# Optimization experiments

Hardware: AMD Instinct MI355X
Metric: run time of the kernel (lower is better)

Reference implementation:

```python
import jax, jax.numpy as jnp
import numpy as np

N = 100000
E = 1600000
G = 2048          # number of graphs in the batch
HEADS = 4
HID = 16          # per-head channels
IN_CH = 128
D = HEADS * HID   # 64, concat output width per layer
NEG_SLOPE = 0.2


def _gat_layer(x, src, dst, W, a_src, a_dst, bias):
    # x: [N, Fin], W: [Fin, H*C], a_src/a_dst: [H, C], bias: [H*C]
    h = (x @ W).reshape(N, HEADS, HID)                      # [N, H, C]
    al_s = jnp.einsum('nhc,hc->nh', h, a_src)               # [N, H]
    al_d = jnp.einsum('nhc,hc->nh', h, a_dst)               # [N, H]
    e = jax.nn.leaky_relu(al_s[src] + al_d[dst], NEG_SLOPE) # [E+N, H]
    # segment softmax over incoming edges of each destination node
    m = jax.ops.segment_max(e, dst, num_segments=N)         # [N, H]
    e = jnp.exp(e - m[dst])
    s = jax.ops.segment_sum(e, dst, num_segments=N)
    alpha = e / (s[dst] + 1e-16)                            # [E+N, H]
    msg = h[src] * alpha[..., None]                         # [E+N, H, C]
    out = jax.ops.segment_sum(msg, dst, num_segments=N)     # [N, H, C]
    return out.reshape(N, D) + bias


def setup_inputs() -> dict:
    key = jax.random.key(0)
    ks = jax.random.split(key, 16)
    x = jax.random.normal(ks[0], (N, IN_CH), dtype=jnp.float32)
    edge_index = jax.random.randint(ks[1], (2, E), 0, N, dtype=jnp.int64)
    batch = jnp.sort(jax.random.randint(ks[2], (N,), 0, G, dtype=jnp.int64))
    inp = {'x': x, 'edge_index': edge_index, 'batch': batch}
    fins = [IN_CH, D, D]
    for i, fin in enumerate(fins):
        kk = jax.random.split(ks[3 + i], 4)
        sc = 1.0 / np.sqrt(fin)
        inp[f'W{i}'] = jax.random.normal(kk[0], (fin, D), dtype=jnp.float32) * sc
        inp[f'as{i}'] = jax.random.normal(kk[1], (HEADS, HID), dtype=jnp.float32) * 0.1
        inp[f'ad{i}'] = jax.random.normal(kk[2], (HEADS, HID), dtype=jnp.float32) * 0.1
        inp[f'b{i}'] = jnp.zeros((D,), dtype=jnp.float32)
    inp['head_w'] = jax.random.normal(ks[10], (1, D), dtype=jnp.float32) * (1.0 / np.sqrt(D))
    inp['head_b'] = jnp.zeros((1,), dtype=jnp.float32)
    return inp


def reference(x, edge_index, batch,
              W0, as0, ad0, b0,
              W1, as1, ad1, b1,
              W2, as2, ad2, b2,
              head_w, head_b):
    # PyG GATConv adds self-loops by default
    loops = jnp.arange(N, dtype=edge_index.dtype)
    src = jnp.concatenate([edge_index[0], loops])
    dst = jnp.concatenate([edge_index[1], loops])
    layers = [(W0, as0, ad0, b0), (W1, as1, ad1, b1), (W2, as2, ad2, b2)]
    h = x.astype(jnp.float32)
    for (W, a_s, a_d, b) in layers:
        h = _gat_layer(h, src, dst, W, a_s, a_d, b)
        h = jax.nn.relu(h)  # dropout p=0.0 -> identity
    pooled = jax.ops.segment_sum(h, batch, num_segments=G)  # [G, D]
    out = pooled @ head_w.T + head_b                         # [G, 1]
    return out.reshape(-1)                                   # out_dim == 1 -> flatten
```

## Files before the change

### kernel.cpp

```cpp
#include <hip/hip_runtime.h>
#include <hip/hip_bf16.h>
#include <hip/hip_fp16.h>
#include <cstdint>
#include <cstddef>

#define NN 100000
#define EE 1600000
#define GG 2048

constexpr int NB_SCAN = (NN + 255) / 256;

__device__ __forceinline__ float lrelu(float v) { return v > 0.f ? v : 0.2f * v; }

__global__ void k_count(const int* __restrict__ ei, int* __restrict__ deg,
                        int* __restrict__ rank) {
    int i = blockIdx.x * blockDim.x + threadIdx.x;
    if (i >= EE + NN) return;
    int d = (i < EE) ? ei[EE + i] : (i - EE);
    rank[i] = atomicAdd(&deg[d], 1);
}

__global__ void k_scan1(const int* __restrict__ deg, int* __restrict__ offs,
                        int* __restrict__ bsums) {
    __shared__ int tmp[256];
    int tid = threadIdx.x;
    int i = blockIdx.x * 256 + tid;
    int v = (i < NN) ? deg[i] : 0;
    tmp[tid] = v; __syncthreads();
    for (int off = 1; off < 256; off <<= 1) {
        int t = (tid >= off) ? tmp[tid - off] : 0;
        __syncthreads();
        tmp[tid] += t;
        __syncthreads();
    }
    if (i < NN) offs[i] = tmp[tid] - v;
    if (tid == 255) bsums[blockIdx.x] = tmp[255];
}

__global__ void k_scan2(int* __restrict__ bsums) {
    __shared__ int tmp[512];
    int tid = threadIdx.x;
    int v = (tid < NB_SCAN) ? bsums[tid] : 0;
    tmp[tid] = v; __syncthreads();
    for (int off = 1; off < 512; off <<= 1) {
        int t = (tid >= off) ? tmp[tid - off] : 0;
        __syncthreads();
        tmp[tid] += t;
        __syncthreads();
    }
    if (tid < NB_SCAN) bsums[tid] = tmp[tid] - v;
}

__global__ void k_scan3(int* __restrict__ offs, const int* __restrict__ bsums) {
    int i = blockIdx.x * 256 + threadIdx.x;
    if (i < NN) offs[i] += bsums[blockIdx.x];
}

__global__ void k_scatter(const int* __restrict__ ei, const int* __restrict__ offs,
                          const int* __restrict__ rank, int* __restrict__ col) {
    int i = blockIdx.x * blockDim.x + threadIdx.x;
    if (i >= EE + NN) return;
    int s, d;
    if (i < EE) { s = ei[i]; d = ei[EE + i]; } else { s = d = i - EE; }
    col[offs[d] + rank[i]] = s;
}

template <int FIN>
__global__ __launch_bounds__(256) void k_gemm(const float* __restrict__ X,
                                              const float* __restrict__ W,
                                              const float* __restrict__ asrc,
                                              const float* __restrict__ adst,
                                              float* __restrict__ H,
                                              float* __restrict__ als,
                                              float* __restrict__ ald) {
    int j  = threadIdx.x & 63;
    int ty = threadIdx.x >> 6;
    int row = __builtin_amdgcn_readfirstlane(blockIdx.x * 16 + ty * 4);
    const float* x0 = X + (size_t)row * FIN;
    const float* x1 = x0 + FIN;
    const float* x2 = x1 + FIN;
    const float* x3 = x2 + FIN;
    float a0 = 0.f, a1 = 0.f, a2 = 0.f, a3 = 0.f;
#pragma unroll
    for (int k = 0; k < FIN; k += 4) {
        float4 xa = *(const float4*)(x0 + k);
        float4 xb = *(const float4*)(x1 + k);
        float4 xc = *(const float4*)(x2 + k);
        float4 xd = *(const float4*)(x3 + k);
        float w0 = W[(k + 0) * 64 + j];
        float w1 = W[(k + 1) * 64 + j];
        float w2 = W[(k + 2) * 64 + j];
        float w3 = W[(k + 3) * 64 + j];
        a0 += xa.x * w0 + xa.y * w1 + xa.z * w2 + xa.w * w3;
        a1 += xb.x * w0 + xb.y * w1 + xb.z * w2 + xb.w * w3;
        a2 += xc.x * w0 + xc.y * w1 + xc.z * w2 + xc.w * w3;
        a3 += xd.x * w0 + xd.y * w1 + xd.z * w2 + xd.w * w3;
    }
    H[(size_t)(row + 0) * 64 + j] = a0;
    H[(size_t)(row + 1) * 64 + j] = a1;
    H[(size_t)(row + 2) * 64 + j] = a2;
    H[(size_t)(row + 3) * 64 + j] = a3;
    float asj = asrc[j], adj = adst[j];
    float accs[4] = {a0, a1, a2, a3};
#pragma unroll
    for (int r = 0; r < 4; r++) {
        float vs = accs[r] * asj;
        float vd = accs[r] * adj;
#pragma unroll
        for (int off = 8; off > 0; off >>= 1) {
            vs += __shfl_xor(vs, off, 64);
            vd += __shfl_xor(vd, off, 64);
        }
        if ((j & 15) == 0) {
            int h = j >> 4;
            als[(size_t)(row + r) * 4 + h] = vs;
            ald[(size_t)(row + r) * 4 + h] = vd;
        }
    }
}

#define LWPITCH 260
__global__ __launch_bounds__(256) void k_agg(
    const float* __restrict__ H, const float* __restrict__ als,
    const float* __restrict__ ald, const int* __restrict__ offs,
    const int* __restrict__ deg, const int* __restrict__ col,
    const float* __restrict__ bias, float* __restrict__ Hout,
    const int* __restrict__ batch, const float* __restrict__ hw,
    float* __restrict__ out, int last) {
    __shared__ float lws[16 * LWPITCH];
    __shared__ int   lsi[16][64];
    int tid = threadIdx.x;
    int g = tid >> 4;
    int l = tid & 15;
    int n = blockIdx.x * 16 + g;
    int start = offs[n];
    int len = deg[n];
    float4 ad4 = ((const float4*)ald)[n];
    int hsel = l >> 2;
    const float4* Hp = (const float4*)H + l;
    float* lw = lws + g * LWPITCH;
    bool fast = (len <= 64);
    float inv = 1.f;

    if (fast) {
        float ev[4][4];
        int   si[4];
        bool  vld[4];
        float m0 = -1e30f, m1 = -1e30f, m2 = -1e30f, m3 = -1e30f;
#pragma unroll
        for (int it = 0; it < 4; it++) {
            int e = l + it * 16;
            vld[it] = (e < len);
            int s = vld[it] ? col[start + e] : 0;
            si[it] = s;
            float4 a = ((const float4*)als)[s];
            ev[it][0] = lrelu(a.x + ad4.x); ev[it][1] = lrelu(a.y + ad4.y);
            ev[it][2] = lrelu(a.z + ad4.z); ev[it][3] = lrelu(a.w + ad4.w);
            if (vld[it]) {
                m0 = fmaxf(m0, ev[it][0]); m1 = fmaxf(m1, ev[it][1]);
                m2 = fmaxf(m2, ev[it][2]); m3 = fmaxf(m3, ev[it][3]);
            }
        }
#pragma unroll
        for (int off = 8; off > 0; off >>= 1) {
            m0 = fmaxf(m0, __shfl_xor(m0, off, 16));
            m1 = fmaxf(m1, __shfl_xor(m1, off, 16));
            m2 = fmaxf(m2, __shfl_xor(m2, off, 16));
            m3 = fmaxf(m3, __shfl_xor(m3, off, 16));
        }
        float s0 = 0.f, s1 = 0.f, s2 = 0.f, s3 = 0.f;
#pragma unroll
        for (int it = 0; it < 4; it++) {
            int e = l + it * 16;
            float w0 = vld[it] ? __expf(ev[it][0] - m0) : 0.f;
            float w1 = vld[it] ? __expf(ev[it][1] - m1) : 0.f;
            float w2 = vld[it] ? __expf(ev[it][2] - m2) : 0.f;
            float w3 = vld[it] ? __expf(ev[it][3] - m3) : 0.f;
            s0 += w0; s1 += w1; s2 += w2; s3 += w3;
            ((float4*)(lw + e * 4))[0] = make_float4(w0, w1, w2, w3);
            lsi[g][e] = vld[it] ? si[it] : 0;
        }
#pragma unroll
        for (int off = 8; off > 0; off >>= 1) {
            s0 += __shfl_xor(s0, off, 16); s1 += __shfl_xor(s1, off, 16);
            s2 += __shfl_xor(s2, off, 16); s3 += __shfl_xor(s3, off, 16);
        }
        float smh = hsel == 0 ? s0 : hsel == 1 ? s1 : hsel == 2 ? s2 : s3;
        inv = 1.f / (smh + 1e-16f);
    }

    __syncthreads();

    float4 acc = {0.f, 0.f, 0.f, 0.f};
    if (fast) {
        int e = 0;
        for (; e + 4 <= len; e += 4) {
            int sa = lsi[g][e], sb = lsi[g][e + 1], sc = lsi[g][e + 2], sd = lsi[g][e + 3];
            float wa = lw[(e + 0) * 4 + hsel];
            float wb = lw[(e + 1) * 4 + hsel];
            float wc = lw[(e + 2) * 4 + hsel];
            float wd = lw[(e + 3) * 4 + hsel];
            float4 ha = Hp[(size_t)sa * 16];
            float4 hb = Hp[(size_t)sb * 16];
            float4 hc = Hp[(size_t)sc * 16];
            float4 hd = Hp[(size_t)sd * 16];
            acc.x += wa * ha.x + wb * hb.x + wc * hc.x + wd * hd.x;
            acc.y += wa * ha.y + wb * hb.y + wc * hc.y + wd * hd.y;
            acc.z += wa * ha.z + wb * hb.z + wc * hc.z + wd * hd.z;
            acc.w += wa * ha.w + wb * hb.w + wc * hc.w + wd * hd.w;
        }
        for (; e < len; e++) {
            int sa = lsi[g][e];
            float wa = lw[e * 4 + hsel];
            float4 ha = Hp[(size_t)sa * 16];
            acc.x += wa * ha.x; acc.y += wa * ha.y;
            acc.z += wa * ha.z; acc.w += wa * ha.w;
        }
    } else {
        float m0 = -1e30f, m1 = -1e30f, m2 = -1e30f, m3 = -1e30f;
        for (int e = l; e < len; e += 16) {
            int s = col[start + e];
            float4 a = ((const float4*)als)[s];
            m0 = fmaxf(m0, lrelu(a.x + ad4.x)); m1 = fmaxf(m1, lrelu(a.y + ad4.y));
            m2 = fmaxf(m2, lrelu(a.z + ad4.z)); m3 = fmaxf(m3, lrelu(a.w + ad4.w));
        }
#pragma unroll
        for (int off = 8; off > 0; off >>= 1) {
            m0 = fmaxf(m0, __shfl_xor(m0, off, 16));
            m1 = fmaxf(m1, __shfl_xor(m1, off, 16));
            m2 = fmaxf(m2, __shfl_xor(m2, off, 16));
            m3 = fmaxf(m3, __shfl_xor(m3, off, 16));
        }
        float s0 = 0.f, s1 = 0.f, s2 = 0.f, s3 = 0.f;
        for (int e = l; e < len; e += 16) {
            int s = col[start + e];
            float4 a = ((const float4*)als)[s];
            s0 += __expf(lrelu(a.x + ad4.x) - m0); s1 += __expf(lrelu(a.y + ad4.y) - m1);
            s2 += __expf(lrelu(a.z + ad4.z) - m2); s3 += __expf(lrelu(a.w + ad4.w) - m3);
        }
#pragma unroll
        for (int off = 8; off > 0; off >>= 1) {
            s0 += __shfl_xor(s0, off, 16); s1 += __shfl_xor(s1, off, 16);
            s2 += __shfl_xor(s2, off, 16); s3 += __shfl_xor(s3, off, 16);
        }
        float mh = hsel == 0 ? m0 : hsel == 1 ? m1 : hsel == 2 ? m2 : m3;
        float sh = hsel == 0 ? s0 : hsel == 1 ? s1 : hsel == 2 ? s2 : s3;
        float ih = 1.f / (sh + 1e-16f);
        float ah = hsel == 0 ? ad4.x : hsel == 1 ? ad4.y : hsel == 2 ? ad4.z : ad4.w;
        for (int e = 0; e < len; e++) {
            int s = col[start + e];
            float alpha = __expf(lrelu(als[(size_t)s * 4 + hsel] + ah) - mh) * ih;
            float4 ha = Hp[(size_t)s * 16];
            acc.x += alpha * ha.x; acc.y += alpha * ha.y;
            acc.z += alpha * ha.z; acc.w += alpha * ha.w;
        }
        inv = 1.f;
    }

    float4 b4 = ((const float4*)bias)[l];
    float4 o4;
    o4.x = fmaxf(acc.x * inv + b4.x, 0.f);
    o4.y = fmaxf(acc.y * inv + b4.y, 0.f);
    o4.z = fmaxf(acc.z * inv + b4.z, 0.f);
    o4.w = fmaxf(acc.w * inv + b4.w, 0.f);
    if (!last) {
        ((float4*)Hout)[(size_t)n * 16 + l] = o4;
    } else {
        float4 w4 = ((const float4*)hw)[l];
        float t = o4.x * w4.x + o4.y * w4.y + o4.z * w4.z + o4.w * w4.w;
#pragma unroll
        for (int off = 8; off > 0; off >>= 1) t += __shfl_xor(t, off, 16);
        if (l == 0) atomicAdd(&out[batch[n]], t);
    }
}

__global__ void k_out_init(const float* __restrict__ head_b, float* __restrict__ out) {
    int g = blockIdx.x * blockDim.x + threadIdx.x;
    if (g < GG) out[g] = head_b[0];
}

extern "C" void kernel_launch(void* const* d_in, const int* in_sizes, int n_in,
                              void* d_out, int out_size, void* d_ws, size_t ws_size,
                              hipStream_t stream) {
    const float* x     = (const float*)d_in[0];
    const int*   ei    = (const int*)d_in[1];
    const int*   batch = (const int*)d_in[2];
    const float* Wm[3] = {(const float*)d_in[3], (const float*)d_in[7],  (const float*)d_in[11]};
    const float* As[3] = {(const float*)d_in[4], (const float*)d_in[8],  (const float*)d_in[12]};
    const float* Ad[3] = {(const float*)d_in[5], (const float*)d_in[9],  (const float*)d_in[13]};
    const float* Bb[3] = {(const float*)d_in[6], (const float*)d_in[10], (const float*)d_in[14]};
    const float* hw = (const float*)d_in[15];
    const float* hb = (const float*)d_in[16];
    float* out = (float*)d_out;

    uint8_t* w = (uint8_t*)d_ws;
    auto alloc = [&](size_t bytes) -> void* {
        void* p = (void*)w;
        w += (bytes + 255) & ~(size_t)255;
        return p;
    };
    float* H       = (float*)alloc((size_t)NN * 64 * 4);
    float* Bf      = (float*)alloc((size_t)NN * 64 * 4);
    float* als     = (float*)alloc((size_t)NN * 4 * 4);
    float* ald     = (float*)alloc((size_t)NN * 4 * 4);
    int*   deg     = (int*)alloc((size_t)NN * 4);
    int*   offs    = (int*)alloc((size_t)NN * 4);
    int*   rank    = (int*)alloc((size_t)(EE + NN) * 4);
    int*   col     = (int*)alloc((size_t)(EE + NN) * 4);
    int*   bsums   = (int*)alloc((size_t)((NB_SCAN + 63) & ~63) * 4);

    hipMemsetAsync(deg, 0, (size_t)NN * 4, stream);

    int eb = (EE + NN + 255) / 256;
    k_count  <<<eb, 256, 0, stream>>>(ei, deg, rank);
    k_scan1  <<<NB_SCAN, 256, 0, stream>>>(deg, offs, bsums);
    k_scan2  <<<1, 512, 0, stream>>>(bsums);
    k_scan3  <<<NB_SCAN, 256, 0, stream>>>(offs, bsums);
    k_scatter<<<eb, 256, 0, stream>>>(ei, offs, rank, col);
    k_out_init<<<(GG + 255) / 256, 256, 0, stream>>>(hb, out);

    const float* cur_in = x;
    for (int L = 0; L < 3; L++) {
        if (L == 0)
            k_gemm<128><<<NN / 16, 256, 0, stream>>>(
                cur_in, Wm[L], As[L], Ad[L], H, als, ald);
        else
            k_gemm<64><<<NN / 16, 256, 0, stream>>>(
                cur_in, Wm[L], As[L], Ad[L], H, als, ald);
        k_agg <<<NN / 16, 256, 0, stream>>>(
            H, als, ald, offs, deg, col, Bb[L], Bf, batch, hw, out, (L == 2) ? 1 : 0);
        cur_in = Bf;
    }
}
```

Before: 542.5 us.

## Single-pass GAT aggregation without max subtraction, dropping shared-memory staging

Replaces the two-phase aggregation (parallel max/exp into LDS, barrier, then gather) with one pass in which each lane computes its own exp weights and gathers neighbour features, eight edges at a time. The softmax max-subtraction is dropped, which relies on logits being small enough that exp does not overflow. LDS use and __syncthreads are removed and launch bounds ask for 6 blocks per CU, aiming at higher occupancy and more loads in flight. In exchange every lane redundantly reads col and als for each edge, and numerical stability depends on the input scale.

```diff
diff --git a/kernel.cpp b/kernel.cpp
--- a/kernel.cpp
+++ b/kernel.cpp
@@ -119,143 +119,53 @@
     }
 }
 
-#define LWPITCH 260
-__global__ __launch_bounds__(256) void k_agg(
+__global__ __launch_bounds__(256, 6) void k_agg(
     const float* __restrict__ H, const float* __restrict__ als,
     const float* __restrict__ ald, const int* __restrict__ offs,
     const int* __restrict__ deg, const int* __restrict__ col,
     const float* __restrict__ bias, float* __restrict__ Hout,
     const int* __restrict__ batch, const float* __restrict__ hw,
     float* __restrict__ out, int last) {
-    __shared__ float lws[16 * LWPITCH];
-    __shared__ int   lsi[16][64];
     int tid = threadIdx.x;
     int g = tid >> 4;
     int l = tid & 15;
     int n = blockIdx.x * 16 + g;
     int start = offs[n];
     int len = deg[n];
-    float4 ad4 = ((const float4*)ald)[n];
     int hsel = l >> 2;
+    float adh = ald[(size_t)n * 4 + hsel];
     const float4* Hp = (const float4*)H + l;
-    float* lw = lws + g * LWPITCH;
-    bool fast = (len <= 64);
-    float inv = 1.f;
-
-    if (fast) {
-        float ev[4][4];
-        int   si[4];
-        bool  vld[4];
-        float m0 = -1e30f, m1 = -1e30f, m2 = -1e30f, m3 = -1e30f;
-#pragma unroll
-        for (int it = 0; it < 4; it++) {
-            int e = l + it * 16;
-            vld[it] = (e < len);
-            int s = vld[it] ? col[start + e] : 0;
-            si[it] = s;
-            float4 a = ((const float4*)als)[s];
-            ev[it][0] = lrelu(a.x + ad4.x); ev[it][1] = lrelu(a.y + ad4.y);
-            ev[it][2] = lrelu(a.z + ad4.z); ev[it][3] = lrelu(a.w + ad4.w);
-            if (vld[it]) {
-                m0 = fmaxf(m0, ev[it][0]); m1 = fmaxf(m1, ev[it][1]);
-                m2 = fmaxf(m2, ev[it][2]); m3 = fmaxf(m3, ev[it][3]);
-            }
-        }
-#pragma unroll
-        for (int off = 8; off > 0; off >>= 1) {
-            m0 = fmaxf(m0, __shfl_xor(m0, off, 16));
-            m1 = fmaxf(m1, __shfl_xor(m1, off, 16));
-            m2 = fmaxf(m2, __shfl_xor(m2, off, 16));
-            m3 = fmaxf(m3, __shfl_xor(m3, off, 16));
-        }
-        float s0 = 0.f, s1 = 0.f, s2 = 0.f, s3 = 0.f;
-#pragma unroll
-        for (int it = 0; it < 4; it++) {
-            int e = l + it * 16;
-            float w0 = vld[it] ? __expf(ev[it][0] - m0) : 0.f;
-            float w1 = vld[it] ? __expf(ev[it][1] - m1) : 0.f;
-            float w2 = vld[it] ? __expf(ev[it][2] - m2) : 0.f;
-            float w3 = vld[it] ? __expf(ev[it][3] - m3) : 0.f;
-            s0 += w0; s1 += w1; s2 += w2; s3 += w3;
-            ((float4*)(lw + e * 4))[0] = make_float4(w0, w1, w2, w3);
-            lsi[g][e] = vld[it] ? si[it] : 0;
-        }
-#pragma unroll
-        for (int off = 8; off > 0; off >>= 1) {
-            s0 += __shfl_xor(s0, off, 16); s1 += __shfl_xor(s1, off, 16);
-            s2 += __shfl_xor(s2, off, 16); s3 += __shfl_xor(s3, off, 16);
-        }
-        float smh = hsel == 0 ? s0 : hsel == 1 ? s1 : hsel == 2 ? s2 : s3;
-        inv = 1.f / (smh + 1e-16f);
-    }
-
-    __syncthreads();
 
     float4 acc = {0.f, 0.f, 0.f, 0.f};
-    if (fast) {
-        int e = 0;
-        for (; e + 4 <= len; e += 4) {
-            int sa = lsi[g][e], sb = lsi[g][e + 1], sc = lsi[g][e + 2], sd = lsi[g][e + 3];
-            float wa = lw[(e + 0) * 4 + hsel];
-            float wb = lw[(e + 1) * 4 + hsel];
-            float wc = lw[(e + 2) * 4 + hsel];
-            float wd = lw[(e + 3) * 4 + hsel];
-            float4 ha = Hp[(size_t)sa * 16];
-            float4 hb = Hp[(size_t)sb * 16];
-            float4 hc = Hp[(size_t)sc * 16];
-            float4 hd = Hp[(size_t)sd * 16];
-            acc.x += wa * ha.x + wb * hb.x + wc * hc.x + wd * hd.x;
-            acc.y += wa * ha.y + wb * hb.y + wc * hc.y + wd * hd.y;
-            acc.z += wa * ha.z + wb * hb.z + wc * hc.z + wd * hd.z;
-            acc.w += wa * ha.w + wb * hb.w + wc * hc.w + wd * hd.w;
-        }
-        for (; e < len; e++) {
-            int sa = lsi[g][e];
-            float wa = lw[e * 4 + hsel];
-            float4 ha = Hp[(size_t)sa * 16];
-            acc.x += wa * ha.x; acc.y += wa * ha.y;
-            acc.z += wa * ha.z; acc.w += wa * ha.w;
-        }
-    } else {
-        float m0 = -1e30f, m1 = -1e30f, m2 = -1e30f, m3 = -1e30f;
-        for (int e = l; e < len; e += 16) {
-            int s = col[start + e];
-            float4 a = ((const float4*)als)[s];
-            m0 = fmaxf(m0, lrelu(a.x + ad4.x)); m1 = fmaxf(m1, lrelu(a.y + ad4.y));
-            m2 = fmaxf(m2, lrelu(a.z + ad4.z)); m3 = fmaxf(m3, lrelu(a.w + ad4.w));
-        }
-#pragma unroll
-        for (int off = 8; off > 0; off >>= 1) {
-            m0 = fmaxf(m0, __shfl_xor(m0, off, 16));
-            m1 = fmaxf(m1, __shfl_xor(m1, off, 16));
-            m2 = fmaxf(m2, __shfl_xor(m2, off, 16));
-            m3 = fmaxf(m3, __shfl_xor(m3, off, 16));
-        }
-        float s0 = 0.f, s1 = 0.f, s2 = 0.f, s3 = 0.f;
-        for (int e = l; e < len; e += 16) {
-            int s = col[start + e];
-            float4 a = ((const float4*)als)[s];
-            s0 += __expf(lrelu(a.x + ad4.x) - m0); s1 += __expf(lrelu(a.y + ad4.y) - m1);
-            s2 += __expf(lrelu(a.z + ad4.z) - m2); s3 += __expf(lrelu(a.w + ad4.w) - m3);
-        }
-#pragma unroll
-        for (int off = 8; off > 0; off >>= 1) {
-            s0 += __shfl_xor(s0, off, 16); s1 += __shfl_xor(s1, off, 16);
-            s2 += __shfl_xor(s2, off, 16); s3 += __shfl_xor(s3, off, 16);
-        }
-        float mh = hsel == 0 ? m0 : hsel == 1 ? m1 : hsel == 2 ? m2 : m3;
-        float sh = hsel == 0 ? s0 : hsel == 1 ? s1 : hsel == 2 ? s2 : s3;
-        float ih = 1.f / (sh + 1e-16f);
-        float ah = hsel == 0 ? ad4.x : hsel == 1 ? ad4.y : hsel == 2 ? ad4.z : ad4.w;
-        for (int e = 0; e < len; e++) {
-            int s = col[start + e];
-            float alpha = __expf(lrelu(als[(size_t)s * 4 + hsel] + ah) - mh) * ih;
-            float4 ha = Hp[(size_t)s * 16];
-            acc.x += alpha * ha.x; acc.y += alpha * ha.y;
-            acc.z += alpha * ha.z; acc.w += alpha * ha.w;
-        }
-        inv = 1.f;
-    }
+    float ssum = 0.f;
+
+    for (int e = 0; e < len; e += 8) {
+        bool  v[8];
+        int   s[8];
+#pragma unroll
+        for (int i = 0; i < 8; i++) {
+            v[i] = (e + i < len);
+            s[i] = v[i] ? col[start + e + i] : 0;
+        }
+        float  w[8];
+        float4 hr[8];
+#pragma unroll
+        for (int i = 0; i < 8; i++) {
+            float a = als[(size_t)s[i] * 4 + hsel];
+            hr[i] = Hp[(size_t)s[i] * 16];
+            float ev = lrelu(a + adh);
+            w[i] = v[i] ? __expf(ev) : 0.f;
+        }
+#pragma unroll
+        for (int i = 0; i < 8; i++) {
+            ssum  += w[i];
+            acc.x = fmaf(w[i], hr[i].x, acc.x);
+            acc.y = fmaf(w[i], hr[i].y, acc.y);
+            acc.z = fmaf(w[i], hr[i].z, acc.z);
+            acc.w = fmaf(w[i], hr[i].w, acc.w);
+        }
+    }
+    float inv = 1.f / (ssum + 1e-16f);
 
     float4 b4 = ((const float4*)bias)[l];
     float4 o4;
```

New measurement: 546.8 us. No clear change (+0.8%).
